# Optimization experiments

Hardware: AMD Instinct MI355X
Metric: run time of the kernel (lower is better)

The kernel has to match this reference:

```python
import jax, jax.numpy as jnp
import numpy as np
import math

D_MODEL = 1024
N_HEADS = 16
C = 1
B, L = 8, 2048


def _glorot(key, fan):
    lim = np.sqrt(6.0 / (fan + fan)).astype(np.float32)
    return jax.random.uniform(key, (fan, fan), jnp.float32, -lim, lim)


def setup_inputs() -> dict:
    key = jax.random.key(0)
    ks = jax.random.split(key, 7)
    queries = jax.random.normal(ks[0], (B, L, D_MODEL), jnp.float32)
    keys = jax.random.normal(ks[1], (B, L, D_MODEL), jnp.float32)
    values = jax.random.normal(ks[2], (B, L, D_MODEL), jnp.float32)
    wq = _glorot(ks[3], D_MODEL)
    wk = _glorot(ks[4], D_MODEL)
    wv = _glorot(ks[5], D_MODEL)
    wo = _glorot(ks[6], D_MODEL)
    return {"queries": queries, "keys": keys, "values": values,
            "wq": wq, "wk": wk, "wv": wv, "wo": wo}


def reference(queries, keys, values, wq, wk, wv, wo):
    Bv, Lv, _ = queries.shape
    H = N_HEADS
    Dh = D_MODEL // N_HEADS
    # Projections, then (B, L, H, Dh) -> (B, H, Dh, L)  (time axis last)
    Q = (queries @ wq).reshape(Bv, Lv, H, Dh).transpose(0, 2, 3, 1)
    K = (keys @ wk).reshape(Bv, Lv, H, Dh).transpose(0, 2, 3, 1)
    V = (values @ wv).reshape(Bv, Lv, H, Dh).transpose(0, 2, 3, 1)
    # FFT-based autocorrelation over the time axis, per (B,H,Dh) lane
    corr = jnp.fft.irfft(jnp.fft.rfft(Q, axis=-1) * jnp.conj(jnp.fft.rfft(K, axis=-1)), n=Lv, axis=-1)  # (B,H,Dh,L)
    k_top = int(math.floor(C * math.log(Lv)))
    top_vals, top_idx = jax.lax.top_k(corr, k_top)          # (B,H,Dh,k)
    w = jax.nn.softmax(top_vals, axis=-1)                    # (B,H,Dh,k)
    # Faithful to original roll_function: it rolls along the Dh axis
    # (which the source mislabels as seq_len), shifts taken mod Dh.
    # out[b,h,t,:] = V[b,h,(t - tau[b,h,t]) % Dh, :]
    t = jnp.arange(Dh)
    out = jnp.zeros_like(V)
    for i in range(k_top):  # small static loop (k_top = 7)
        gather_idx = (t[None, None, :] - top_idx[..., i]) % Dh   # (B,H,Dh)
        rolled = jnp.take_along_axis(V, gather_idx[..., None], axis=2)  # (B,H,Dh,L)
        out = out + w[..., i, None] * rolled
    # Faithful layout-scrambling reshape: (B,H,Dh,L)->(B,Dh,H,L)->(B,L,d_model)
    out = out.transpose(0, 2, 1, 3).reshape(Bv, Lv, D_MODEL)
    return out @ wo
```

## Files before the change

kernel.cpp:

```cpp
#include <hip/hip_runtime.h>
#include <math.h>

#define NB 8
#define NL 2048
#define ND 1024
#define NH 16
#define KTOP 7

typedef __attribute__((ext_vector_type(4))) float f32x4;
typedef __attribute__((ext_vector_type(8))) short s16x8;
typedef __attribute__((ext_vector_type(8))) _Float16 f16x8;
typedef __attribute__((ext_vector_type(4))) _Float16 f16x4;

__device__ __forceinline__ unsigned short f2bf(float x) {
  unsigned u = __float_as_uint(x);
  u = (u + 0x7FFFu + ((u >> 16) & 1u)) >> 16;
  return (unsigned short)u;
}
__device__ __forceinline__ float bf2f(unsigned short h) {
  return __uint_as_float(((unsigned)h) << 16);
}
__device__ __forceinline__ unsigned cvtpk_bf16(float a, float b) {
  unsigned d;
  asm("v_cvt_pk_bf16_f32 %0, %1, %2" : "=v"(d) : "v"(a), "v"(b));
  return d;
}
__device__ __forceinline__ float lo16(unsigned h) { return __uint_as_float(h << 16); }
__device__ __forceinline__ float hi16(unsigned h) { return __uint_as_float(h & 0xffff0000u); }

__device__ __forceinline__ void gll16(const void* g, void* l) {
  __builtin_amdgcn_global_load_lds(
      (const __attribute__((address_space(1))) void*)g,
      (__attribute__((address_space(3))) void*)l, 16, 0, 0);
}

__device__ __forceinline__ void asplit_write(float4 x, float4 y, short* ah, short* al, int wi) {
  unsigned h0 = cvtpk_bf16(x.x, x.y);
  unsigned h1 = cvtpk_bf16(x.z, x.w);
  unsigned h2 = cvtpk_bf16(y.x, y.y);
  unsigned h3 = cvtpk_bf16(y.z, y.w);
  float r0 = x.x - lo16(h0), r1 = x.y - hi16(h0);
  float r2 = x.z - lo16(h1), r3 = x.w - hi16(h1);
  float r4 = y.x - lo16(h2), r5 = y.y - hi16(h2);
  float r6 = y.z - lo16(h3), r7 = y.w - hi16(h3);
  unsigned l0 = cvtpk_bf16(r0, r1);
  unsigned l1 = cvtpk_bf16(r2, r3);
  unsigned l2 = cvtpk_bf16(r4, r5);
  unsigned l3 = cvtpk_bf16(r6, r7);
  *(uint4*)(ah + wi) = make_uint4(h0, h1, h2, h3);
  *(uint4*)(al + wi) = make_uint4(l0, l1, l2, l3);
}

__global__ __launch_bounds__(256) void wprep_kernel(
    const float* __restrict__ w0, const float* __restrict__ w1,
    const float* __restrict__ w2, const float* __restrict__ w3,
    short* __restrict__ wsplit, _Float16* __restrict__ wf16) {
  __shared__ float tile[32][33];
  int y = blockIdx.y;
  const float* in = (y == 0) ? w0 : (y == 1) ? w1 : (y == 2) ? w2 : w3;
  int bx = blockIdx.x & 31, by = blockIdx.x >> 5;
  int tx = threadIdx.x & 31, ty = threadIdx.x >> 5;
#pragma unroll
  for (int i = 0; i < 4; ++i)
    tile[ty + i * 8][tx] = in[(size_t)(by * 32 + ty + i * 8) * ND + bx * 32 + tx];
  __syncthreads();
#pragma unroll
  for (int i = 0; i < 4; ++i) {
    float x = tile[tx][ty + i * 8];
    int n = bx * 32 + ty + i * 8;
    int k = by * 32 + tx;
    if (y < 2) {
      short* oh = wsplit + (size_t)(2 * y) * ND * ND;
      short* ol = wsplit + (size_t)(2 * y + 1) * ND * ND;
      unsigned short h = f2bf(x);
      unsigned short l = f2bf(x - bf2f(h));
      size_t o = (size_t)n * ND + (k ^ (((n >> 1) & 3) << 3));
      oh[o] = (short)h;
      ol[o] = (short)l;
    } else {
      _Float16* of = wf16 + (size_t)(y - 2) * ND * ND;
      of[(size_t)n * ND + (k ^ ((n & 7) << 3))] = (_Float16)x;
    }
  }
}

__global__ __launch_bounds__(256) void gemm_split(
    const float* __restrict__ A, const short* __restrict__ BhT,
    const short* __restrict__ BlT, float* __restrict__ Ct) {
  constexpr int K = 1024;
  __shared__ short smem[32768];
  int t = threadIdx.x;
  int wg = (blockIdx.x & 7) * 128 + (blockIdx.x >> 3);
  int m0 = (wg >> 3) << 7, n0 = (wg & 7) << 7;
  int lane = t & 63;
  int wm = (t >> 7) & 1, wn = (t >> 6) & 1;
  int lrow = lane & 15, lk8 = (lane >> 4) << 3;

  int r0 = t >> 2, r1 = r0 + 64;
  int c8 = (t & 3) << 3;
  int wi0 = r0 * 32 + (c8 ^ (((r0 >> 1) & 3) << 3));
  int wi1 = r1 * 32 + (c8 ^ (((r1 >> 1) & 3) << 3));
  int lo0 = (t & 192) * 8;
  int lo1 = 2048 + (t & 192) * 8;

  const float* pa0 = A + (size_t)(m0 + r0) * K + c8;
  const float* pa1 = A + (size_t)(m0 + r1) * K + c8;
  const short* pb0h = BhT + (size_t)(n0 + r0) * K + c8;
  const short* pb1h = BhT + (size_t)(n0 + r1) * K + c8;
  const short* pb0l = BlT + (size_t)(n0 + r0) * K + c8;
  const short* pb1l = BlT + (size_t)(n0 + r1) * K + c8;

  int iA[4], iB[4];
#pragma unroll
  for (int f = 0; f < 4; ++f) {
    int ra = wm * 64 + f * 16 + lrow;
    iA[f] = ra * 32 + (lk8 ^ (((ra >> 1) & 3) << 3));
    int rb = wn * 64 + f * 16 + lrow;
    iB[f] = rb * 32 + (lk8 ^ (((rb >> 1) & 3) << 3));
  }

  f32x4 acc[4][4] = {};

  float4 sx0 = *(const float4*)(pa0);
  float4 sy0 = *(const float4*)(pa0 + 4);
  float4 sx1 = *(const float4*)(pa1);
  float4 sy1 = *(const float4*)(pa1 + 4);
  gll16(pb0h, smem + 8192 + lo0);
  gll16(pb1h, smem + 8192 + lo1);
  gll16(pb0l, smem + 12288 + lo0);
  gll16(pb1l, smem + 12288 + lo1);
  asplit_write(sx0, sy0, smem, smem + 4096, wi0);
  asplit_write(sx1, sy1, smem, smem + 4096, wi1);
  __syncthreads();

  for (int k0 = 0; k0 < K; k0 += 32) {
    short* cb = smem + ((k0 >> 5) & 1) * 16384;
    short* nb = smem + ((((k0 >> 5) & 1) ^ 1) * 16384);
    bool more = (k0 + 32) < K;
    if (more) {
      sx0 = *(const float4*)(pa0 + k0 + 32);
      sy0 = *(const float4*)(pa0 + k0 + 36);
      sx1 = *(const float4*)(pa1 + k0 + 32);
      sy1 = *(const float4*)(pa1 + k0 + 36);
      gll16(pb0h + k0 + 32, nb + 8192 + lo0);
      gll16(pb1h + k0 + 32, nb + 8192 + lo1);
      gll16(pb0l + k0 + 32, nb + 12288 + lo0);
      gll16(pb1l + k0 + 32, nb + 12288 + lo1);
    }
    s16x8 afh[4], afl[4];
#pragma unroll
    for (int mf = 0; mf < 4; ++mf) {
      afh[mf] = *(const s16x8*)(cb + iA[mf]);
      afl[mf] = *(const s16x8*)(cb + 4096 + iA[mf]);
    }
#pragma unroll
    for (int nf = 0; nf < 4; ++nf) {
      s16x8 bfh = *(const s16x8*)(cb + 8192 + iB[nf]);
      s16x8 bfl = *(const s16x8*)(cb + 12288 + iB[nf]);
#pragma unroll
      for (int mf = 0; mf < 4; ++mf)
        acc[mf][nf] = __builtin_amdgcn_mfma_f32_16x16x32_bf16(afh[mf], bfh, acc[mf][nf], 0, 0, 0);
#pragma unroll
      for (int mf = 0; mf < 4; ++mf)
        acc[mf][nf] = __builtin_amdgcn_mfma_f32_16x16x32_bf16(afh[mf], bfl, acc[mf][nf], 0, 0, 0);
#pragma unroll
      for (int mf = 0; mf < 4; ++mf)
        acc[mf][nf] = __builtin_amdgcn_mfma_f32_16x16x32_bf16(afl[mf], bfh, acc[mf][nf], 0, 0, 0);
    }
    if (more) {
      asplit_write(sx0, sy0, nb, nb + 4096, wi0);
      asplit_write(sx1, sy1, nb, nb + 4096, wi1);
    }
    __syncthreads();
  }

  int b = m0 >> 11;
  int mlbase = (m0 & 2047) + wm * 64 + (lane >> 4) * 4;
#pragma unroll
  for (int nf = 0; nf < 4; ++nf) {
    int n = n0 + wn * 64 + nf * 16 + lrow;
    float* rowp = Ct + ((size_t)(b * ND + n)) * NL + mlbase;
#pragma unroll
    for (int mf = 0; mf < 4; ++mf)
      *(float4*)(rowp + mf * 16) = *(float4*)&acc[mf][nf];
  }
}

template <int OUTMODE, bool AF32>
__global__ __launch_bounds__(256) void gemm_f16(
    const void* __restrict__ Av, const _Float16* __restrict__ BT,
    void* __restrict__ Cv) {
  constexpr int K = 1024;
  __shared__ _Float16 smem[32768];
  int t = threadIdx.x;
  int wg = (blockIdx.x & 7) * 128 + (blockIdx.x >> 3);
  int m0 = (wg >> 3) << 7, n0 = (wg & 7) << 7;
  int lane = t & 63;
  int wm = (t >> 7) & 1, wn = (t >> 6) & 1;
  int lrow = lane & 15, lk = (lane >> 4) << 3;

  int rs = t >> 3;
  int c8 = (t & 7) << 3;
  const _Float16* pB[4];
  const float* pAf[4];
  const _Float16* pAh[4];
  int wiA[4], lo[4];
#pragma unroll
  for (int it = 0; it < 4; ++it) {
    int r = it * 32 + rs;
    pB[it] = BT + (size_t)(n0 + r) * K + c8;
    lo[it] = it * 2048 + (t & 192) * 8;
    if (AF32) {
      pAf[it] = (const float*)Av + (size_t)(m0 + r) * K + c8;
      wiA[it] = r * 64 + (c8 ^ ((r & 7) << 3));
    } else {
      pAh[it] = (const _Float16*)Av + (size_t)(m0 + r) * K + c8;
    }
  }

  f32x4 acc[4][4] = {};
  float4 ax[4], ay[4];

#pragma unroll
  for (int it = 0; it < 4; ++it) {
    gll16(pB[it], smem + 8192 + lo[it]);
    if (!AF32) {
      gll16(pAh[it], smem + lo[it]);
    } else {
      ax[it] = *(const float4*)(pAf[it]);
      ay[it] = *(const float4*)(pAf[it] + 4);
    }
  }
  if (AF32) {
#pragma unroll
    for (int it = 0; it < 4; ++it) {
      f16x8 o;
      o[0] = (_Float16)ax[it].x; o[1] = (_Float16)ax[it].y;
      o[2] = (_Float16)ax[it].z; o[3] = (_Float16)ax[it].w;
      o[4] = (_Float16)ay[it].x; o[5] = (_Float16)ay[it].y;
      o[6] = (_Float16)ay[it].z; o[7] = (_Float16)ay[it].w;
      *(f16x8*)(smem + wiA[it]) = o;
    }
  }
  __syncthreads();

  for (int k0 = 0; k0 < K; k0 += 64) {
    _Float16* cb = smem + ((k0 >> 6) & 1) * 16384;
    _Float16* nb = smem + ((((k0 >> 6) & 1) ^ 1) * 16384);
    bool more = (k0 + 64) < K;
    if (more) {
#pragma unroll
      for (int it = 0; it < 4; ++it) {
        gll16(pB[it] + k0 + 64, nb + 8192 + lo[it]);
        if (!AF32) {
          gll16(pAh[it] + k0 + 64, nb + lo[it]);
        } else {
          ax[it] = *(const float4*)(pAf[it] + k0 + 64);
          ay[it] = *(const float4*)(pAf[it] + k0 + 68);
        }
      }
    }
#pragma unroll
    for (int kk = 0; kk < 64; kk += 32) {
      f16x8 af[4];
#pragma unroll
      for (int mf = 0; mf < 4; ++mf) {
        int row = wm * 64 + mf * 16 + lrow;
        af[mf] = *(const f16x8*)(cb + row * 64 + ((kk + lk) ^ ((row & 7) << 3)));
      }
#pragma unroll
      for (int nf = 0; nf < 4; ++nf) {
        int row = wn * 64 + nf * 16 + lrow;
        f16x8 bf = *(const f16x8*)(cb + 8192 + row * 64 + ((kk + lk) ^ ((row & 7) << 3)));
#pragma unroll
        for (int mf = 0; mf < 4; ++mf)
          acc[mf][nf] = __builtin_amdgcn_mfma_f32_16x16x32_f16(af[mf], bf, acc[mf][nf], 0, 0, 0);
      }
    }
    if (more && AF32) {
#pragma unroll
      for (int it = 0; it < 4; ++it) {
        f16x8 o;
        o[0] = (_Float16)ax[it].x; o[1] = (_Float16)ax[it].y;
        o[2] = (_Float16)ax[it].z; o[3] = (_Float16)ax[it].w;
        o[4] = (_Float16)ay[it].x; o[5] = (_Float16)ay[it].y;
        o[6] = (_Float16)ay[it].z; o[7] = (_Float16)ay[it].w;
        *(f16x8*)(nb + wiA[it]) = o;
      }
    }
    __syncthreads();
  }

  if (OUTMODE == 0) {
    _Float16* C = (_Float16*)Cv;
    int b = m0 >> 11;
    int ml = (m0 & 2047) + wm * 64 + (lane >> 4) * 4;
#pragma unroll
    for (int nf = 0; nf < 4; ++nf) {
      int n = n0 + wn * 64 + nf * 16 + lrow;
      _Float16* row = C + ((size_t)(b * ND + n)) * NL + ml;
#pragma unroll
      for (int mf = 0; mf < 4; ++mf) {
        f16x4 v;
        v[0] = (_Float16)acc[mf][nf][0];
        v[1] = (_Float16)acc[mf][nf][1];
        v[2] = (_Float16)acc[mf][nf][2];
        v[3] = (_Float16)acc[mf][nf][3];
        *(f16x4*)(row + mf * 16) = v;
      }
    }
  } else {
    float* C = (float*)Cv;
#pragma unroll
    for (int mf = 0; mf < 4; ++mf)
#pragma unroll
      for (int nf = 0; nf < 4; ++nf) {
        int row = m0 + wm * 64 + mf * 16 + (lane >> 4) * 4;
        int col = n0 + wn * 64 + nf * 16 + lrow;
#pragma unroll
        for (int r = 0; r < 4; ++r)
          C[(size_t)(row + r) * ND + col] = acc[mf][nf][r];
      }
  }
}

__device__ __forceinline__ int SW(int i) { return i ^ ((i >> 4) & 7); }

__device__ __forceinline__ float2 cadd2(float2 a, float2 b) { return make_float2(a.x + b.x, a.y + b.y); }
__device__ __forceinline__ float2 csub2(float2 a, float2 b) { return make_float2(a.x - b.x, a.y - b.y); }
__device__ __forceinline__ float2 cmul2(float2 a, float2 b) {
  return make_float2(a.x * b.x - a.y * b.y, a.x * b.y + a.y * b.x);
}
__device__ __forceinline__ float2 cjs2(float2 a, float s) { return make_float2(-s * a.y, s * a.x); }
__device__ __forceinline__ float2 wtw(float rev) {
  return make_float2(__builtin_amdgcn_cosf(rev), __builtin_amdgcn_sinf(rev));
}

__device__ __forceinline__ void dft4(float2& b0, float2& b1, float2& b2, float2& b3, float s) {
  float2 t0 = cadd2(b0, b2), t1 = csub2(b0, b2);
  float2 t2 = cadd2(b1, b3), t3 = cjs2(csub2(b1, b3), s);
  b0 = cadd2(t0, t2);
  b1 = cadd2(t1, t3);
  b2 = csub2(t0, t2);
  b3 = csub2(t1, t3);
}

__device__ __forceinline__ void dft8(float2 a[8], float s) {
  float2 e0 = a[0], e1 = a[2], e2 = a[4], e3 = a[6];
  float2 o0 = a[1], o1 = a[3], o2 = a[5], o3 = a[7];
  dft4(e0, e1, e2, e3, s);
  dft4(o0, o1, o2, o3, s);
  const float c = 0.70710678118654752f;
  float2 w1 = make_float2(c, s * c);
  float2 w3 = make_float2(-c, s * c);
  o1 = cmul2(o1, w1);
  o2 = cjs2(o2, s);
  o3 = cmul2(o3, w3);
  a[0] = cadd2(e0, o0);
  a[4] = csub2(e0, o0);
  a[1] = cadd2(e1, o1);
  a[5] = csub2(e1, o1);
  a[2] = cadd2(e2, o2);
  a[6] = csub2(e2, o2);
  a[3] = cadd2(e3, o3);
  a[7] = csub2(e3, o3);
}

template <int LS>
__device__ __forceinline__ void pass8(const float2* __restrict__ in, float2* __restrict__ out,
                                      float s, int t) {
  float2 a[8];
  const float2* ip = in + (t ^ ((t >> 4) & 7));
#pragma unroll
  for (int r = 0; r < 8; ++r) a[r] = ip[256 * r];
  int k = t & (LS - 1);
  if (LS > 1) {
    float kf = s * (1.0f / (LS * 8)) * (float)k;
    float2 w1 = wtw(kf);
    float2 w4 = wtw(4.0f * kf);
    float2 w2 = cmul2(w1, w1);
    float2 w3 = cmul2(w2, w1);
    float2 w5 = cmul2(w4, w1);
    float2 w6 = cmul2(w4, w2);
    float2 w7 = cmul2(w4, w3);
    a[1] = cmul2(a[1], w1);
    a[2] = cmul2(a[2], w2);
    a[3] = cmul2(a[3], w3);
    a[4] = cmul2(a[4], w4);
    a[5] = cmul2(a[5], w5);
    a[6] = cmul2(a[6], w6);
    a[7] = cmul2(a[7], w7);
  }
  dft8(a, s);
  int ob = (t / LS) * (LS * 8) + k;
#pragma unroll
  for (int r = 0; r < 8; ++r) out[SW(ob + LS * r)] = a[r];
}

__global__ __launch_bounds__(256) void fft_topk_kernel(
    const float* __restrict__ Qt, const float* __restrict__ Kt,
    float* __restrict__ topw, int* __restrict__ topi) {
  __shared__ float2 X[2048];
  __shared__ float2 Y[2048];
  __shared__ float cv[2][4];
  __shared__ int ct[2][4];

  int t = threadIdx.x;
  size_t rix = blockIdx.x;
  const float* q = Qt + rix * NL;
  const float* k = Kt + rix * NL;

#pragma unroll
  for (int it = 0; it < 2; ++it) {
    int i0 = 4 * t + 1024 * it;
    float4 vq = *(const float4*)(q + i0);
    float4 vk = *(const float4*)(k + i0);
    int swb = SW(i0);
    X[swb ^ 0] = make_float2(vq.x, vk.x);
    X[swb ^ 1] = make_float2(vq.y, vk.y);
    X[swb ^ 2] = make_float2(vq.z, vk.z);
    X[swb ^ 3] = make_float2(vq.w, vk.w);
  }
  __syncthreads();

  pass8<1>(X, Y, -1.0f, t);
  __syncthreads();
  pass8<8>(Y, X, -1.0f, t);
  __syncthreads();
  pass8<64>(X, Y, -1.0f, t);
  __syncthreads();
#pragma unroll
  for (int h = 0; h < 2; ++h) {
    int b = t + 256 * h;
    float2 a[4];
    const float2* yp = Y + SW(b);
#pragma unroll
    for (int r = 0; r < 4; ++r) a[r] = yp[512 * r];
    float2 w = wtw(-(1.0f / 2048.0f) * (float)b);
    float2 w2 = cmul2(w, w);
    a[1] = cmul2(a[1], w);
    a[2] = cmul2(a[2], w2);
    a[3] = cmul2(a[3], cmul2(w2, w));
    dft4(a[0], a[1], a[2], a[3], -1.0f);
    float2* xp = X + SW(b);
#pragma unroll
    for (int r = 0; r < 4; ++r) xp[512 * r] = a[r];
  }
  __syncthreads();

  {
    float2 a[8];
    int swt = SW(t);
#pragma unroll
    for (int r = 0; r < 8; ++r) {
      int f = t + 256 * r;
      int nf = (2048 - f) & 2047;
      float2 zf = X[swt + 256 * r];
      float2 zn = X[SW(nf)];
      float aa = zf.x, b2 = zf.y, c = zn.x, d = zn.y;
      float p = 0.5f * (aa + c), qq = 0.5f * (b2 - d);
      float r2 = 0.5f * (b2 + d), s2 = -0.5f * (aa - c);
      a[r] = make_float2((p * r2 + qq * s2) * (1.0f / 2048.0f),
                         (qq * r2 - p * s2) * (1.0f / 2048.0f));
    }
    dft8(a, 1.0f);
    int ob = t * 8;
#pragma unroll
    for (int r = 0; r < 8; ++r) Y[SW(ob + r)] = a[r];
  }
  __syncthreads();

  pass8<8>(Y, X, 1.0f, t);
  __syncthreads();
  pass8<64>(X, Y, 1.0f, t);
  __syncthreads();

  float lv[8];
  int lt[8];
#pragma unroll
  for (int h = 0; h < 2; ++h) {
    int b = t + 256 * h;
    float2 a[4];
    const float2* yp = Y + SW(b);
#pragma unroll
    for (int r = 0; r < 4; ++r) a[r] = yp[512 * r];
    float2 w = wtw((1.0f / 2048.0f) * (float)b);
    float2 w2 = cmul2(w, w);
    a[1] = cmul2(a[1], w);
    a[2] = cmul2(a[2], w2);
    a[3] = cmul2(a[3], cmul2(w2, w));
    dft4(a[0], a[1], a[2], a[3], 1.0f);
#pragma unroll
    for (int r = 0; r < 4; ++r) {
      lv[h * 4 + r] = a[r].x;
      lt[h * 4 + r] = b + 512 * r;
    }
  }

  int lane = t & 63, wave = t >> 6;
  float bv = lv[0];
  int bt = lt[0];
#pragma unroll
  for (int j = 1; j < 8; ++j)
    if (lv[j] > bv) { bv = lv[j]; bt = lt[j]; }

  float sel_v[KTOP];
  int sel_t[KTOP];
#pragma unroll
  for (int pass = 0; pass < KTOP; ++pass) {
    float rv = bv;
    int rt = bt;
#pragma unroll
    for (int m = 1; m < 64; m <<= 1) {
      float ov = __shfl_xor(rv, m, 64);
      int ot = __shfl_xor(rt, m, 64);
      if (ov > rv) { rv = ov; rt = ot; }
    }
    if (lane == 0) { cv[pass & 1][wave] = rv; ct[pass & 1][wave] = rt; }
    __syncthreads();
    float fv = cv[pass & 1][0];
    int ft = ct[pass & 1][0];
#pragma unroll
    for (int w = 1; w < 4; ++w) {
      float ov = cv[pass & 1][w];
      if (ov > fv) { fv = ov; ft = ct[pass & 1][w]; }
    }
    sel_v[pass] = fv;
    sel_t[pass] = ft;
    if (bt == ft) {
#pragma unroll
      for (int j = 0; j < 8; ++j)
        if (lt[j] == ft) lv[j] = -3.0e38f;
      bv = lv[0];
      bt = lt[0];
#pragma unroll
      for (int j = 1; j < 8; ++j)
        if (lv[j] > bv) { bv = lv[j]; bt = lt[j]; }
    }
  }

  if (t == 0) {
    float m = sel_v[0], ssum = 0.f, w[KTOP];
#pragma unroll
    for (int i = 0; i < KTOP; ++i) { w[i] = expf(sel_v[i] - m); ssum += w[i]; }
#pragma unroll
    for (int i = 0; i < KTOP; ++i) {
      topw[rix * KTOP + i] = w[i] / ssum;
      topi[rix * KTOP + i] = sel_t[i];
    }
  }
}

__global__ __launch_bounds__(256) void roll_kernel(
    const _Float16* __restrict__ V, const float* __restrict__ topw,
    const int* __restrict__ topi, _Float16* __restrict__ out) {
  __shared__ float vt[64][68];
  __shared__ float ws[64][8];
  __shared__ int ts[64][8];
  int blk = blockIdx.x;
  int b = blk >> 9;
  int h = (blk >> 5) & 15;
  int lc = blk & 31;
  int t = threadIdx.x;

#pragma unroll
  for (int it = 0; it < 2; ++it) {
    int e = it * 256 + t;
    int d = e >> 3, c8 = (e & 7) << 3;
    f16x8 v = *(const f16x8*)(V + ((size_t)(b * ND + h * 64 + d)) * NL + lc * 64 + c8);
#pragma unroll
    for (int j = 0; j < 8; ++j) vt[d][c8 + j] = (float)v[j];
  }
  for (int e = t; e < 64 * KTOP; e += 256) {
    int d = e / KTOP, i = e % KTOP;
    size_t rix = ((size_t)(b * 16 + h)) * 64 + d;
    ws[d][i] = topw[rix * KTOP + i];
    ts[d][i] = topi[rix * KTOP + i] & 63;
  }
  __syncthreads();

  int hi = lc >> 4;
  int c0 = (lc & 15) * 64;
#pragma unroll
  for (int it = 0; it < 16; ++it) {
    int e = it * 256 + t;
    int d = e >> 6, r = e & 63;
    float s = 0.f;
#pragma unroll
    for (int i = 0; i < KTOP; ++i) s += ws[d][i] * vt[(d - ts[d][i]) & 63][r];
    int rowp = d * 32 + h * 2 + hi;
    int col = c0 + r;
    out[((size_t)(b * NL + rowp)) * ND + (col ^ ((rowp & 7) << 3))] = (_Float16)s;
  }
}

extern "C" void kernel_launch(void* const* d_in, const int* in_sizes, int n_in,
                              void* d_out, int out_size, void* d_ws, size_t ws_size,
                              hipStream_t stream) {
  (void)in_sizes; (void)n_in; (void)out_size; (void)ws_size;
  const float* queries = (const float*)d_in[0];
  const float* keys    = (const float*)d_in[1];
  const float* values  = (const float*)d_in[2];
  const float* wq = (const float*)d_in[3];
  const float* wk = (const float*)d_in[4];
  const float* wv = (const float*)d_in[5];
  const float* wo = (const float*)d_in[6];
  float* outp = (float*)d_out;

  const size_t MB = 1024 * 1024;
  char* ws = (char*)d_ws;
  short*    wsplit = (short*)ws;
  _Float16* wf16   = (_Float16*)(ws + 8 * MB);
  float*    Qt     = (float*)(ws + 12 * MB);
  float*    Kt     = (float*)(ws + 76 * MB);
  float*    topw   = (float*)(ws + 140 * MB);
  int*      topi   = (int*)(ws + 140 * MB + (size_t)8192 * KTOP * 4);

  short* wqh = wsplit + (size_t)0 * ND * ND;
  short* wql = wsplit + (size_t)1 * ND * ND;
  short* wkh = wsplit + (size_t)2 * ND * ND;
  short* wkl = wsplit + (size_t)3 * ND * ND;
  _Float16* wv16 = wf16 + (size_t)0 * ND * ND;
  _Float16* wo16 = wf16 + (size_t)1 * ND * ND;

  _Float16* Vp = (_Float16*)Qt;
  _Float16* Xs = (_Float16*)Kt;

  wprep_kernel<<<dim3(1024, 4), 256, 0, stream>>>(wq, wk, wv, wo, wsplit, wf16);

  gemm_split<<<1024, 256, 0, stream>>>(queries, wqh, wql, Qt);
  gemm_split<<<1024, 256, 0, stream>>>(keys, wkh, wkl, Kt);

  fft_topk_kernel<<<8192, 256, 0, stream>>>(Qt, Kt, topw, topi);

  gemm_f16<0, true><<<1024, 256, 0, stream>>>(values, wv16, Vp);

  roll_kernel<<<NB * NH * 32, 256, 0, stream>>>(Vp, topw, topi, Xs);

  gemm_f16<2, false><<<1024, 256, 0, stream>>>(Xs, wo16, outp);
}
```

Before: 457.5 us.

## Triple-buffer B tiles in split GEMM with partial vmcnt barrier

Restructures the split-bf16 projection GEMM so the B (weight) tiles are loaded two iterations ahead into a three-slot LDS ring, while the A tiles keep a double buffer. The barrier waits only until at most 4 vector memory ops are outstanding, letting the next B tile's direct-to-LDS loads stay in flight across the barrier. This is meant to hide global load latency better, at the cost of more LDS per block, which may reduce occupancy, and redundant clamped loads on the last iterations.

```diff
diff --git a/kernel.cpp b/kernel.cpp
--- a/kernel.cpp
+++ b/kernel.cpp
@@ -51,6 +51,8 @@
   *(uint4*)(al + wi) = make_uint4(l0, l1, l2, l3);
 }
 
+#define BARRIER_VM4() asm volatile("s_waitcnt vmcnt(4) lgkmcnt(0)\n\ts_barrier" ::: "memory")
+
 __global__ __launch_bounds__(256) void wprep_kernel(
     const float* __restrict__ w0, const float* __restrict__ w1,
     const float* __restrict__ w2, const float* __restrict__ w3,
@@ -88,7 +90,7 @@
     const float* __restrict__ A, const short* __restrict__ BhT,
     const short* __restrict__ BlT, float* __restrict__ Ct) {
   constexpr int K = 1024;
-  __shared__ short smem[32768];
+  __shared__ short smem[40960];
   int t = threadIdx.x;
   int wg = (blockIdx.x & 7) * 128 + (blockIdx.x >> 3);
   int m0 = (wg >> 3) << 7, n0 = (wg & 7) << 7;
@@ -121,42 +123,52 @@
 
   f32x4 acc[4][4] = {};
 
-  float4 sx0 = *(const float4*)(pa0);
-  float4 sy0 = *(const float4*)(pa0 + 4);
-  float4 sx1 = *(const float4*)(pa1);
-  float4 sy1 = *(const float4*)(pa1 + 4);
-  gll16(pb0h, smem + 8192 + lo0);
-  gll16(pb1h, smem + 8192 + lo1);
-  gll16(pb0l, smem + 12288 + lo0);
-  gll16(pb1l, smem + 12288 + lo1);
-  asplit_write(sx0, sy0, smem, smem + 4096, wi0);
-  asplit_write(sx1, sy1, smem, smem + 4096, wi1);
-  __syncthreads();
-
-  for (int k0 = 0; k0 < K; k0 += 32) {
-    short* cb = smem + ((k0 >> 5) & 1) * 16384;
-    short* nb = smem + ((((k0 >> 5) & 1) ^ 1) * 16384);
-    bool more = (k0 + 32) < K;
-    if (more) {
-      sx0 = *(const float4*)(pa0 + k0 + 32);
-      sy0 = *(const float4*)(pa0 + k0 + 36);
-      sx1 = *(const float4*)(pa1 + k0 + 32);
-      sy1 = *(const float4*)(pa1 + k0 + 36);
-      gll16(pb0h + k0 + 32, nb + 8192 + lo0);
-      gll16(pb1h + k0 + 32, nb + 8192 + lo1);
-      gll16(pb0l + k0 + 32, nb + 12288 + lo0);
-      gll16(pb1l + k0 + 32, nb + 12288 + lo1);
-    }
+  {
+    float4 sx0 = *(const float4*)(pa0);
+    float4 sy0 = *(const float4*)(pa0 + 4);
+    float4 sx1 = *(const float4*)(pa1);
+    float4 sy1 = *(const float4*)(pa1 + 4);
+    gll16(pb0h, smem + 16384 + lo0);
+    gll16(pb1h, smem + 16384 + lo1);
+    gll16(pb0l, smem + 20480 + lo0);
+    gll16(pb1l, smem + 20480 + lo1);
+    gll16(pb0h + 32, smem + 24576 + lo0);
+    gll16(pb1h + 32, smem + 24576 + lo1);
+    gll16(pb0l + 32, smem + 28672 + lo0);
+    gll16(pb1l + 32, smem + 28672 + lo1);
+    asplit_write(sx0, sy0, smem, smem + 4096, wi0);
+    asplit_write(sx1, sy1, smem, smem + 4096, wi1);
+  }
+  BARRIER_VM4();
+
+  int abuf = 0, bbuf = 0;
+  for (int i = 0; i < 32; ++i) {
+    int k0 = i * 32;
+    int kA = (k0 + 32 < K) ? (k0 + 32) : (K - 32);
+    int kB = (k0 + 64 < K) ? (k0 + 64) : (K - 32);
+    int bn2 = bbuf + 2; if (bn2 >= 3) bn2 -= 3;
+    short* aw = smem + (abuf ^ 1) * 8192;
+    short* bw = smem + 16384 + bn2 * 8192;
+    float4 sx0 = *(const float4*)(pa0 + kA);
+    float4 sy0 = *(const float4*)(pa0 + kA + 4);
+    float4 sx1 = *(const float4*)(pa1 + kA);
+    float4 sy1 = *(const float4*)(pa1 + kA + 4);
+    gll16(pb0h + kB, bw + lo0);
+    gll16(pb1h + kB, bw + lo1);
+    gll16(pb0l + kB, bw + 4096 + lo0);
+    gll16(pb1l + kB, bw + 4096 + lo1);
+    short* ca = smem + abuf * 8192;
+    short* cbB = smem + 16384 + bbuf * 8192;
     s16x8 afh[4], afl[4];
 #pragma unroll
     for (int mf = 0; mf < 4; ++mf) {
-      afh[mf] = *(const s16x8*)(cb + iA[mf]);
-      afl[mf] = *(const s16x8*)(cb + 4096 + iA[mf]);
+      afh[mf] = *(const s16x8*)(ca + iA[mf]);
+      afl[mf] = *(const s16x8*)(ca + 4096 + iA[mf]);
     }
 #pragma unroll
     for (int nf = 0; nf < 4; ++nf) {
-      s16x8 bfh = *(const s16x8*)(cb + 8192 + iB[nf]);
-      s16x8 bfl = *(const s16x8*)(cb + 12288 + iB[nf]);
+      s16x8 bfh = *(const s16x8*)(cbB + iB[nf]);
+      s16x8 bfl = *(const s16x8*)(cbB + 4096 + iB[nf]);
 #pragma unroll
       for (int mf = 0; mf < 4; ++mf)
         acc[mf][nf] = __builtin_amdgcn_mfma_f32_16x16x32_bf16(afh[mf], bfh, acc[mf][nf], 0, 0, 0);
@@ -167,11 +179,11 @@
       for (int mf = 0; mf < 4; ++mf)
         acc[mf][nf] = __builtin_amdgcn_mfma_f32_16x16x32_bf16(afl[mf], bfh, acc[mf][nf], 0, 0, 0);
     }
-    if (more) {
-      asplit_write(sx0, sy0, nb, nb + 4096, wi0);
-      asplit_write(sx1, sy1, nb, nb + 4096, wi1);
-    }
-    __syncthreads();
+    asplit_write(sx0, sy0, aw, aw + 4096, wi0);
+    asplit_write(sx1, sy1, aw, aw + 4096, wi1);
+    BARRIER_VM4();
+    abuf ^= 1;
+    bbuf = (bbuf == 2) ? 0 : bbuf + 1;
   }
 
   int b = m0 >> 11;
```

Result: slower. 502.4 us (+9.8%).

## Fuse roll/weighted-gather into V projection GEMM epilogue

Applied to the files above, without the earlier changes.

The V projection GEMM now stages its 128x128 fp32 tile in shared memory and applies the top-k weighted roll along the head dimension directly in the epilogue, writing the scrambled layout consumed by the output GEMM. This removes the separate roll kernel and the fp16 V intermediate round trip through global memory. In exchange the GEMM epilogue grows, adds shared memory for the weights and indices plus an extra sync, and may raise register pressure.

```diff
diff --git a/kernel.cpp b/kernel.cpp
--- a/kernel.cpp
+++ b/kernel.cpp
@@ -189,9 +189,11 @@
 template <int OUTMODE, bool AF32>
 __global__ __launch_bounds__(256) void gemm_f16(
     const void* __restrict__ Av, const _Float16* __restrict__ BT,
-    void* __restrict__ Cv) {
+    void* __restrict__ Cv, const float* __restrict__ topw, const int* __restrict__ topi) {
   constexpr int K = 1024;
   __shared__ _Float16 smem[32768];
+  __shared__ float wls[128][KTOP];
+  __shared__ int tls[128][KTOP];
   int t = threadIdx.x;
   int wg = (blockIdx.x & 7) * 128 + (blockIdx.x >> 3);
   int m0 = (wg >> 3) << 7, n0 = (wg & 7) << 7;
@@ -308,6 +310,55 @@
         v[3] = (_Float16)acc[mf][nf][3];
         *(f16x4*)(row + mf * 16) = v;
       }
+    }
+  } else if (OUTMODE == 1) {
+    float* ct = (float*)smem;
+#pragma unroll
+    for (int nf = 0; nf < 4; ++nf) {
+      int nl = wn * 64 + nf * 16 + lrow;
+#pragma unroll
+      for (int mf = 0; mf < 4; ++mf) {
+        int ml = wm * 64 + (lane >> 4) * 4 + mf * 16;
+        int cc = (((ml >> 2) ^ (nl & 7)) << 2);
+        *(float4*)(ct + nl * 128 + cc) = *(float4*)&acc[mf][nf];
+      }
+    }
+    int b = m0 >> 11;
+    int h0 = n0 >> 6;
+    for (int e = t; e < 128 * KTOP; e += 256) {
+      int nl = e / KTOP, i = e - nl * KTOP;
+      size_t rix = ((size_t)(b * 16 + h0 + (nl >> 6))) * 64 + (nl & 63);
+      wls[nl][i] = topw[rix * KTOP + i];
+      tls[nl][i] = topi[rix * KTOP + i] & 63;
+    }
+    __syncthreads();
+
+    int hi = (m0 >> 10) & 1;
+    int cbase = (m0 & 2047) & 1023;
+    _Float16* O = (_Float16*)Cv;
+#pragma unroll
+    for (int it2 = 0; it2 < 16; ++it2) {
+      int o = it2 * 1024 + t * 4;
+      int lr = o >> 7;
+      int c4 = o & 127;
+      int d = lr >> 1, hl = lr & 1;
+      int wrow = hl * 64 + d;
+      float4 s = {0.f, 0.f, 0.f, 0.f};
+#pragma unroll
+      for (int i = 0; i < KTOP; ++i) {
+        int sr = hl * 64 + ((d - tls[wrow][i]) & 63);
+        float w = wls[wrow][i];
+        int scc = (((c4 >> 2) ^ (sr & 7)) << 2);
+        float4 v = *(const float4*)(ct + sr * 128 + scc);
+        s.x += w * v.x; s.y += w * v.y; s.z += w * v.z; s.w += w * v.w;
+      }
+      int rowp = d * 32 + (h0 + hl) * 2 + hi;
+      int cg = cbase + c4;
+      int cs = cg ^ ((rowp & 7) << 3);
+      f16x4 v4;
+      v4[0] = (_Float16)s.x; v4[1] = (_Float16)s.y;
+      v4[2] = (_Float16)s.z; v4[3] = (_Float16)s.w;
+      *(f16x4*)(O + ((size_t)(b * NL + rowp)) * ND + cs) = v4;
     }
   } else {
     float* C = (float*)Cv;
@@ -551,49 +602,6 @@
   }
 }
 
-__global__ __launch_bounds__(256) void roll_kernel(
-    const _Float16* __restrict__ V, const float* __restrict__ topw,
-    const int* __restrict__ topi, _Float16* __restrict__ out) {
-  __shared__ float vt[64][68];
-  __shared__ float ws[64][8];
-  __shared__ int ts[64][8];
-  int blk = blockIdx.x;
-  int b = blk >> 9;
-  int h = (blk >> 5) & 15;
-  int lc = blk & 31;
-  int t = threadIdx.x;
-
-#pragma unroll
-  for (int it = 0; it < 2; ++it) {
-    int e = it * 256 + t;
-    int d = e >> 3, c8 = (e & 7) << 3;
-    f16x8 v = *(const f16x8*)(V + ((size_t)(b * ND + h * 64 + d)) * NL + lc * 64 + c8);
-#pragma unroll
-    for (int j = 0; j < 8; ++j) vt[d][c8 + j] = (float)v[j];
-  }
-  for (int e = t; e < 64 * KTOP; e += 256) {
-    int d = e / KTOP, i = e % KTOP;
-    size_t rix = ((size_t)(b * 16 + h)) * 64 + d;
-    ws[d][i] = topw[rix * KTOP + i];
-    ts[d][i] = topi[rix * KTOP + i] & 63;
-  }
-  __syncthreads();
-
-  int hi = lc >> 4;
-  int c0 = (lc & 15) * 64;
-#pragma unroll
-  for (int it = 0; it < 16; ++it) {
-    int e = it * 256 + t;
-    int d = e >> 6, r = e & 63;
-    float s = 0.f;
-#pragma unroll
-    for (int i = 0; i < KTOP; ++i) s += ws[d][i] * vt[(d - ts[d][i]) & 63][r];
-    int rowp = d * 32 + h * 2 + hi;
-    int col = c0 + r;
-    out[((size_t)(b * NL + rowp)) * ND + (col ^ ((rowp & 7) << 3))] = (_Float16)s;
-  }
-}
-
 extern "C" void kernel_launch(void* const* d_in, const int* in_sizes, int n_in,
                               void* d_out, int out_size, void* d_ws, size_t ws_size,
                               hipStream_t stream) {
@@ -623,7 +631,6 @@
   _Float16* wv16 = wf16 + (size_t)0 * ND * ND;
   _Float16* wo16 = wf16 + (size_t)1 * ND * ND;
 
-  _Float16* Vp = (_Float16*)Qt;
   _Float16* Xs = (_Float16*)Kt;
 
   wprep_kernel<<<dim3(1024, 4), 256, 0, stream>>>(wq, wk, wv, wo, wsplit, wf16);
@@ -633,9 +640,7 @@
 
   fft_topk_kernel<<<8192, 256, 0, stream>>>(Qt, Kt, topw, topi);
 
-  gemm_f16<0, true><<<1024, 256, 0, stream>>>(values, wv16, Vp);
-
-  roll_kernel<<<NB * NH * 32, 256, 0, stream>>>(Vp, topw, topi, Xs);
-
-  gemm_f16<2, false><<<1024, 256, 0, stream>>>(Xs, wo16, outp);
-}
+  gemm_f16<1, true><<<1024, 256, 0, stream>>>(values, wv16, Xs, topw, topi);
+
+  gemm_f16<2, false><<<1024, 256, 0, stream>>>(Xs, wo16, outp, nullptr, nullptr);
+}
```

Result: faster. 443.4 us (-3.1%).
